# Kernel tuning notes

Hardware: AMD Instinct MI355X
Metric: run time of the kernel (lower is better)

## Reference

```python
import jax, jax.numpy as jnp
import numpy as np

N = 200_000      # n_reflns
NIMG = 500       # n_images
DMETA = 24       # metadata features
WIDTH = 32       # mlp_width
HID = 64         # hidden_units = 2*width (FeedForward default)
DEPTH = 20       # mlp_depth
NPOST = 2        # Normal posterior: (loc, scale)
EPS = 1e-12
KLW = 0.01       # scaling_kl_weight


def setup_inputs() -> dict:
    key = jax.random.key(0)
    ks = jax.random.split(key, 10)
    metadata = jax.random.normal(ks[0], (N, DMETA), jnp.float32)
    iobs = jax.random.normal(ks[1], (N, 1), jnp.float32)
    sigiobs = jax.random.uniform(ks[2], (N, 1), jnp.float32)
    image_ids = jnp.sort(jax.random.randint(ks[3], (N,), 0, NIMG)).astype(jnp.int32)
    n_reflns_per_image = jnp.bincount(image_ids, length=NIMG).astype(jnp.int32)
    d_img = DMETA + 2  # concat(metadata, iobs, sigiobs)
    w_img_in = jax.random.normal(ks[4], (d_img, WIDTH), jnp.float32) / np.float32(np.sqrt(d_img))
    b_img_in = jnp.zeros((WIDTH,), jnp.float32)
    w_scale_in = jax.random.normal(ks[5], (DMETA, WIDTH), jnp.float32) / np.float32(np.sqrt(DMETA))
    b_scale_in = jnp.zeros((WIDTH,), jnp.float32)
    # shared residual FeedForward stack (share_weights=True): x + W2 @ relu(W1 @ x)
    mlp_w1 = jax.random.normal(ks[6], (DEPTH, WIDTH, HID), jnp.float32) / np.float32(np.sqrt(WIDTH))
    mlp_b1 = jnp.zeros((DEPTH, HID), jnp.float32)
    mlp_w2 = jax.random.normal(ks[7], (DEPTH, HID, WIDTH), jnp.float32) * np.float32(0.1 / np.sqrt(HID))
    mlp_b2 = jnp.zeros((DEPTH, WIDTH), jnp.float32)
    w_out = jax.random.normal(ks[8], (WIDTH, NPOST), jnp.float32) / np.float32(np.sqrt(WIDTH))
    b_out = jnp.zeros((NPOST,), jnp.float32)
    return {
        'metadata': metadata, 'iobs': iobs, 'sigiobs': sigiobs,
        'w_img_in': w_img_in, 'b_img_in': b_img_in,
        'w_scale_in': w_scale_in, 'b_scale_in': b_scale_in,
        'mlp_w1': mlp_w1, 'mlp_b1': mlp_b1, 'mlp_w2': mlp_w2, 'mlp_b2': mlp_b2,
        'w_out': w_out, 'b_out': b_out,
        'image_ids_in_this_batch': image_ids,
        'n_reflns_per_image': n_reflns_per_image,
        'mc_samples': 32,
    }


def _mlp(h, w1, b1, w2, b2):
    # depth residual FF blocks, weights stacked along leading DEPTH axis
    def block(h, ws):
        wa, ba, wb, bb = ws
        h = h + (jax.nn.relu(h @ wa + ba) @ wb + bb)
        return h, None
    h, _ = jax.lax.scan(block, h, (w1, b1, w2, b2))
    return h


def reference(metadata, iobs, sigiobs,
              w_img_in, b_img_in, w_scale_in, b_scale_in,
              mlp_w1, mlp_b1, mlp_w2, mlp_b2, w_out, b_out,
              image_ids_in_this_batch, n_reflns_per_image, mc_samples):
    image = jnp.concatenate([metadata, iobs, sigiobs], axis=-1)   # (N, DMETA+2)
    h = image @ w_img_in + b_img_in                               # (N, W)
    h = _mlp(h, mlp_w1, mlp_b1, mlp_w2, mlp_b2)
    nimg = n_reflns_per_image.shape[0]
    sums = jax.ops.segment_sum(h, image_ids_in_this_batch, num_segments=nimg)
    counts = jnp.maximum(n_reflns_per_image, 1).astype(h.dtype)[:, None]
    pooled = sums / counts                                        # (NIMG, W) image-average pool
    s = metadata @ w_scale_in + b_scale_in + pooled[image_ids_in_this_batch]
    s = _mlp(s, mlp_w1, mlp_b1, mlp_w2, mlp_b2)                   # shared weights
    params = s @ w_out + b_out                                    # (N, 2)
    loc = params[:, 0]
    scale = jax.nn.softplus(params[:, 1]) + EPS
    # rsample from Normal(loc, scale), mc_samples draws
    noise = jax.random.normal(jax.random.key(42), (mc_samples, loc.shape[0]), loc.dtype)
    z = loc + scale * noise                                       # (S, N)
    # MC KL estimate: mean_s[log q(z) - log p(z)], p = Laplace(0, 1)
    log_q = -0.5 * jnp.square(noise) - jnp.log(scale) - np.float32(0.5 * np.log(2.0 * np.pi))
    log_p = -jnp.abs(z) - np.float32(np.log(2.0))
    kl_div = KLW * jnp.mean(log_q - log_p, axis=0)                # (N,)
    return z.T, kl_div
```

## Files before the change

### kernel.cpp

```cpp
#include <hip/hip_runtime.h>
#include <stdint.h>

#define N_ROWS 200000
#define NIMG   500
#define DMETA  24
#define WIDTH  32
#define HID    64
#define DEPTH  20
#define MC     32

#define LSTRIDE_F 68
#define TILE_F    (16 * LSTRIDE_F)

#define WB    64000
#define LSTR  17920
#define OFF_WIH (WB + DEPTH * LSTR)
#define OFF_WIL (OFF_WIH + 2048)
#define OFF_WSH (OFF_WIH + 4096)
#define OFF_WSL (OFF_WIH + 6144)

typedef __attribute__((ext_vector_type(8))) short bf16x8;
typedef __attribute__((ext_vector_type(4))) float f32x4;

#define MFMA(a, b, acc) __builtin_amdgcn_mfma_f32_16x16x32_bf16((a), (b), (acc), 0, 0, 0)

__device__ __forceinline__ uint32_t rotl32(uint32_t x, int r) {
    return (x << r) | (x >> (32 - r));
}

__device__ __forceinline__ uint32_t tf_bits(uint32_t j) {
    const uint32_t ks1 = 42u, ks2 = 0x1BD11BDAu ^ 42u;
    uint32_t x0 = 0u, x1 = j + ks1;
#define R4(a,b,c,d) \
    x0 += x1; x1 = rotl32(x1,(a)); x1 ^= x0; \
    x0 += x1; x1 = rotl32(x1,(b)); x1 ^= x0; \
    x0 += x1; x1 = rotl32(x1,(c)); x1 ^= x0; \
    x0 += x1; x1 = rotl32(x1,(d)); x1 ^= x0;
    R4(13,15,26,6)  x0 += ks1; x1 += ks2 + 1u;
    R4(17,29,16,24) x0 += ks2; x1 += 0u + 2u;
    R4(13,15,26,6)                x1 += ks1 + 3u;
    R4(17,29,16,24) x0 += ks1; x1 += ks2 + 4u;
    R4(13,15,26,6)  x0 += ks2; x1 += 0u + 5u;
#undef R4
    return x0 ^ x1;
}

__device__ __forceinline__ float bits_to_normal(uint32_t b) {
    float f = __uint_as_float((b >> 9) | 0x3f800000u) - 1.0f;
    const float lo = -0.99999994f;
    float u = fmaxf(lo, f * 2.0f + lo);
    return 1.41421356f * erfinvf(u);
}

__device__ __forceinline__ void split1(float x, short& hi, short& lo) {
    uint32_t b = __float_as_uint(x);
    uint32_t a = b + 0x8000u;
    hi = (short)(a >> 16);
    float r = x - __uint_as_float(a & 0xFFFF0000u);
    lo = (short)(__float_as_uint(r) >> 16);
}

__device__ __forceinline__ void split8p(const float* x, bf16x8& hi, bf16x8& lo) {
    uint32_t hu[4], lu[4];
#pragma unroll
    for (int p = 0; p < 4; ++p) {
        float x0 = x[2 * p], x1 = x[2 * p + 1];
        uint32_t h;
        asm("v_cvt_pk_bf16_f32 %0, %1, %2" : "=v"(h) : "v"(x0), "v"(x1));
        float r0 = x0 - __uint_as_float(h << 16);
        float r1 = x1 - __uint_as_float(h & 0xFFFF0000u);
        uint32_t l;
        asm("v_cvt_pk_bf16_f32 %0, %1, %2" : "=v"(l) : "v"(r0), "v"(r1));
        hu[p] = h;
        lu[p] = l;
    }
    __builtin_memcpy(&hi, hu, 16);
    __builtin_memcpy(&lo, lu, 16);
}

__device__ __forceinline__ void mlp20_x2(
    float* hC0, float* hC1, float* smw, const char* __restrict__ wsb,
    int lane, int q, int c) {
    const int ldsR = c * LSTRIDE_F + q * 8;
    const int ldsW = q * 4 * LSTRIDE_F + c;
    uint32_t offA  = (uint32_t)(WB + (lane << 4));
    uint32_t offB  = offA + 4096u;
    uint32_t offC  = offA + 8192u;
    uint32_t offD  = offA + 12288u;
    uint32_t offB1 = (uint32_t)(WB + 16384 + (c << 4));
    uint32_t offB2 = (uint32_t)(WB + 17408 + (c << 4));
#pragma unroll 1
    for (int l = 0; l < DEPTH; ++l) {
#pragma unroll
        for (int t = 0; t < 2; ++t)
#pragma unroll
            for (int r = 0; r < 4; ++r) {
                smw[ldsW + r * LSTRIDE_F + t * 16] = hC0[t * 4 + r];
                smw[TILE_F + ldsW + r * LSTRIDE_F + t * 16] = hC1[t * 4 + r];
            }
        f32x4 v0 = *(const f32x4*)(smw + ldsR);
        f32x4 v1 = *(const f32x4*)(smw + ldsR + 4);
        f32x4 u0 = *(const f32x4*)(smw + TILE_F + ldsR);
        f32x4 u1 = *(const f32x4*)(smw + TILE_F + ldsR + 4);
        float a0[8], a1[8];
#pragma unroll
        for (int j = 0; j < 4; ++j) {
            a0[j] = v0[j]; a0[4 + j] = v1[j];
            a1[j] = u0[j]; a1[4 + j] = u1[j];
        }
        bf16x8 ah0, al0, ah1, al1;
        split8p(a0, ah0, al0);
        split8p(a1, ah1, al1);
        float C1v0[16], C1v1[16];
#pragma unroll
        for (int t = 0; t < 4; ++t) {
            uint32_t o = (t < 2 ? offA : offB) + (uint32_t)((t & 1) << 11);
            bf16x8 bh = *(const bf16x8*)(wsb + o);
            bf16x8 bl = *(const bf16x8*)(wsb + o + 1024);
            f32x4 b1q = *(const f32x4*)(wsb + offB1 + (uint32_t)(t << 8));
            f32x4 acc = MFMA(ah0, bh, b1q);
            acc = MFMA(ah0, bl, acc); acc = MFMA(al0, bh, acc);
            f32x4 acd = MFMA(ah1, bh, b1q);
            acd = MFMA(ah1, bl, acd); acd = MFMA(al1, bh, acd);
#pragma unroll
            for (int r = 0; r < 4; ++r) {
                C1v0[t * 4 + r] = fmaxf(acc[r], 0.0f);
                C1v1[t * 4 + r] = fmaxf(acd[r], 0.0f);
            }
        }
#pragma unroll
        for (int t = 0; t < 4; ++t)
#pragma unroll
            for (int r = 0; r < 4; ++r) {
                smw[ldsW + r * LSTRIDE_F + t * 16] = C1v0[t * 4 + r];
                smw[TILE_F + ldsW + r * LSTRIDE_F + t * 16] = C1v1[t * 4 + r];
            }
        f32x4 b2q0 = *(const f32x4*)(wsb + offB2);
        f32x4 b2q1 = *(const f32x4*)(wsb + offB2 + 256u);
        f32x4 acc0[2], acc1[2];
#pragma unroll
        for (int r = 0; r < 4; ++r) {
            acc0[0][r] = hC0[r] + b2q0[r];
            acc0[1][r] = hC0[4 + r] + b2q1[r];
            acc1[0][r] = hC1[r] + b2q0[r];
            acc1[1][r] = hC1[4 + r] + b2q1[r];
        }
#pragma unroll
        for (int kf = 0; kf < 2; ++kf) {
            f32x4 e0a = *(const f32x4*)(smw + ldsR + kf * 32);
            f32x4 e0b = *(const f32x4*)(smw + ldsR + kf * 32 + 4);
            f32x4 e1a = *(const f32x4*)(smw + TILE_F + ldsR + kf * 32);
            f32x4 e1b = *(const f32x4*)(smw + TILE_F + ldsR + kf * 32 + 4);
            float e0[8], e1[8];
#pragma unroll
            for (int j = 0; j < 4; ++j) {
                e0[j] = e0a[j]; e0[4 + j] = e0b[j];
                e1[j] = e1a[j]; e1[4 + j] = e1b[j];
            }
            bf16x8 xh0, xl0, xh1, xl1;
            split8p(e0, xh0, xl0);
            split8p(e1, xh1, xl1);
#pragma unroll
            for (int t2 = 0; t2 < 2; ++t2) {
                uint32_t o = (kf ? offD : offC) + (uint32_t)(t2 << 11);
                bf16x8 bh = *(const bf16x8*)(wsb + o);
                bf16x8 bl = *(const bf16x8*)(wsb + o + 1024);
                acc0[t2] = MFMA(xh0, bh, acc0[t2]);
                acc0[t2] = MFMA(xh0, bl, acc0[t2]);
                acc0[t2] = MFMA(xl0, bh, acc0[t2]);
                acc1[t2] = MFMA(xh1, bh, acc1[t2]);
                acc1[t2] = MFMA(xh1, bl, acc1[t2]);
                acc1[t2] = MFMA(xl1, bh, acc1[t2]);
            }
        }
#pragma unroll
        for (int t2 = 0; t2 < 2; ++t2)
#pragma unroll
            for (int r = 0; r < 4; ++r) {
                hC0[t2 * 4 + r] = acc0[t2][r];
                hC1[t2 * 4 + r] = acc1[t2][r];
            }
        offA += LSTR; offB += LSTR; offC += LSTR; offD += LSTR;
        offB1 += LSTR; offB2 += LSTR;
    }
}

__device__ __forceinline__ void input_proj(
    const bf16x8& ah, const bf16x8& al, const short* __restrict__ wfh,
    const short* __restrict__ wfl, const float* __restrict__ bias,
    float* hC, int lane, int c) {
#pragma unroll
    for (int t = 0; t < 2; ++t) {
        bf16x8 bh = *(const bf16x8*)(wfh + ((t << 9) + (lane << 3)));
        bf16x8 bl = *(const bf16x8*)(wfl + ((t << 9) + (lane << 3)));
        float bb = bias[16 * t + c];
        f32x4 acc = {bb, bb, bb, bb};
        acc = MFMA(ah, bh, acc); acc = MFMA(ah, bl, acc); acc = MFMA(al, bh, acc);
#pragma unroll
        for (int r = 0; r < 4; ++r) hC[t * 4 + r] = acc[r];
    }
}

__global__ __launch_bounds__(256) void prep_kernel(
    const float* __restrict__ w1, const float* __restrict__ w2,
    const float* __restrict__ wimg, const float* __restrict__ wsc,
    const float* __restrict__ b1, const float* __restrict__ b2,
    char* __restrict__ wsb) {
    int t = blockIdx.x * 256 + threadIdx.x;
    float* sums = (float*)wsb;
    if (t < 16000) { sums[t] = 0.0f; return; }
    t -= 16000;
    if (t < 40960) {
        int l = t >> 11, r = t & 2047, tt = r >> 9, r2 = r & 511;
        int lane = r2 >> 3, j = r2 & 7;
        int k = (lane >> 4) * 8 + j, n = 16 * tt + (lane & 15);
        short h, lo;
        split1(w1[l * 2048 + k * 64 + n], h, lo);
        char* base = wsb + WB + l * LSTR + tt * 2048 + 2 * r2;
        *(short*)(base) = h;
        *(short*)(base + 1024) = lo;
        return;
    }
    t -= 40960;
    if (t < 40960) {
        int l = t >> 11, r = t & 2047, kf = r >> 10, r2 = r & 1023;
        int t2 = r2 >> 9, r3 = r2 & 511, lane = r3 >> 3, j = r3 & 7;
        int k = kf * 32 + (lane >> 4) * 8 + j, n = 16 * t2 + (lane & 15);
        short h, lo;
        split1(w2[l * 2048 + k * 32 + n], h, lo);
        char* base = wsb + WB + l * LSTR + 8192 + (kf * 2 + t2) * 2048 + 2 * r3;
        *(short*)(base) = h;
        *(short*)(base + 1024) = lo;
        return;
    }
    t -= 40960;
    if (t < 1024) {
        int tt = t >> 9, r = t & 511, lane = r >> 3, j = r & 7;
        int k = (lane >> 4) * 8 + j, n = 16 * tt + (lane & 15);
        float v = (k < 26) ? wimg[k * 32 + n] : 0.0f;
        short h, lo;
        split1(v, h, lo);
        ((short*)(wsb + OFF_WIH))[t] = h;
        ((short*)(wsb + OFF_WIL))[t] = lo;
        return;
    }
    t -= 1024;
    if (t < 1024) {
        int tt = t >> 9, r = t & 511, lane = r >> 3, j = r & 7;
        int k = (lane >> 4) * 8 + j, n = 16 * tt + (lane & 15);
        float v = (k < 24) ? wsc[k * 32 + n] : 0.0f;
        short h, lo;
        split1(v, h, lo);
        ((short*)(wsb + OFF_WSH))[t] = h;
        ((short*)(wsb + OFF_WSL))[t] = lo;
        return;
    }
    t -= 1024;
    if (t < 5120) {
        int l = t >> 8, r = t & 255;
        int tt = r >> 6, cc = (r >> 2) & 15;
        *(float*)(wsb + WB + l * LSTR + 16384 + 4 * r) = b1[l * 64 + tt * 16 + cc];
        return;
    }
    t -= 5120;
    if (t < 2560) {
        int l = t >> 7, r = t & 127;
        int t2 = r >> 6, cc = (r >> 2) & 15;
        *(float*)(wsb + WB + l * LSTR + 17408 + 4 * r) = b2[l * 32 + t2 * 16 + cc];
        return;
    }
}

__device__ __forceinline__ void load_xfrag(
    const float* __restrict__ md, const float* __restrict__ iobs,
    const float* __restrict__ sig, int base, int q, int c,
    bf16x8& ah, bf16x8& al) {
    float xa[8];
    if (q < 3) {
        const f32x4* rp = (const f32x4*)(md + (size_t)(base + c) * DMETA + q * 8);
        f32x4 v0 = rp[0], v1 = rp[1];
#pragma unroll
        for (int j = 0; j < 4; ++j) { xa[j] = v0[j]; xa[4 + j] = v1[j]; }
    } else {
        xa[0] = iobs ? iobs[base + c] : 0.0f;
        xa[1] = sig ? sig[base + c] : 0.0f;
#pragma unroll
        for (int j = 2; j < 8; ++j) xa[j] = 0.0f;
    }
    split8p(xa, ah, al);
}

__global__ __launch_bounds__(128, 4) void pass_a(
    const float* __restrict__ md, const float* __restrict__ iobs,
    const float* __restrict__ sig, const float* __restrict__ bimg,
    const char* __restrict__ wsb, const int* __restrict__ ids,
    float* __restrict__ sums) {
    __shared__ __attribute__((aligned(16))) float smat[2][2 * TILE_F];
    int lane = threadIdx.x & 63, w = threadIdx.x >> 6;
    int q = lane >> 4, c = lane & 15;
    int i0 = (blockIdx.x * 2 + w) * 32;
    float* smw = &smat[w][0];

    bf16x8 ah0, al0, ah1, al1;
    load_xfrag(md, iobs, sig, i0, q, c, ah0, al0);
    load_xfrag(md, iobs, sig, i0 + 16, q, c, ah1, al1);

    float hC0[8], hC1[8];
    input_proj(ah0, al0, (const short*)(wsb + OFF_WIH), (const short*)(wsb + OFF_WIL),
               bimg, hC0, lane, c);
    input_proj(ah1, al1, (const short*)(wsb + OFF_WIH), (const short*)(wsb + OFF_WIL),
               bimg, hC1, lane, c);

    mlp20_x2(hC0, hC1, smw, wsb, lane, q, c);

#pragma unroll
    for (int tile = 0; tile < 2; ++tile) {
        const float* hC = tile ? hC1 : hC0;
        int tb = i0 + tile * 16;
        bool uni = (ids[tb] == ids[tb + 15]);
        if (uni) {
            int id = ids[tb];
#pragma unroll
            for (int t = 0; t < 2; ++t) {
                float s = (hC[t * 4 + 0] + hC[t * 4 + 1]) + (hC[t * 4 + 2] + hC[t * 4 + 3]);
                s += __shfl_xor(s, 16, 64);
                s += __shfl_xor(s, 32, 64);
                if (q == 0) atomicAdd(&sums[id * 32 + 16 * t + c], s);
            }
        } else {
            int idv[4];
#pragma unroll
            for (int r = 0; r < 4; ++r) idv[r] = ids[tb + q * 4 + r];
#pragma unroll
            for (int t = 0; t < 2; ++t)
#pragma unroll
                for (int r = 0; r < 4; ++r)
                    atomicAdd(&sums[idv[r] * 32 + 16 * t + c], hC[t * 4 + r]);
        }
    }
}

__global__ __launch_bounds__(256) void normalize_kernel(float* __restrict__ sums,
                                                        const int* __restrict__ cnts) {
    int t = blockIdx.x * 256 + threadIdx.x;
    if (t < NIMG * WIDTH) {
        int img = t >> 5;
        float cc = (float)max(cnts[img], 1);
        sums[t] = sums[t] / cc;
    }
}

__global__ __launch_bounds__(128, 4) void pass_b(
    const float* __restrict__ md, const float* __restrict__ bsc,
    const char* __restrict__ wsb, const float* __restrict__ wout,
    const float* __restrict__ bout, const int* __restrict__ ids,
    const float* __restrict__ pooled, float* __restrict__ out) {
    __shared__ __attribute__((aligned(16))) float smat[2][2 * TILE_F];
    __shared__ float sls[2][64];
    int lane = threadIdx.x & 63, w = threadIdx.x >> 6;
    int q = lane >> 4, c = lane & 15;
    int i0 = (blockIdx.x * 2 + w) * 32;
    float* smw = &smat[w][0];

    bf16x8 ah0, al0, ah1, al1;
    load_xfrag(md, nullptr, nullptr, i0, q, c, ah0, al0);
    load_xfrag(md, nullptr, nullptr, i0 + 16, q, c, ah1, al1);

    float hC0[8], hC1[8];
    input_proj(ah0, al0, (const short*)(wsb + OFF_WSH), (const short*)(wsb + OFF_WSL),
               bsc, hC0, lane, c);
    input_proj(ah1, al1, (const short*)(wsb + OFF_WSH), (const short*)(wsb + OFF_WSL),
               bsc, hC1, lane, c);
#pragma unroll
    for (int tile = 0; tile < 2; ++tile) {
        float* hC = tile ? hC1 : hC0;
        int tb = i0 + tile * 16;
        int idv[4];
#pragma unroll
        for (int r = 0; r < 4; ++r) idv[r] = ids[tb + q * 4 + r];
#pragma unroll
        for (int t = 0; t < 2; ++t)
#pragma unroll
            for (int r = 0; r < 4; ++r)
                hC[t * 4 + r] += pooled[idv[r] * 32 + 16 * t + c];
    }

    mlp20_x2(hC0, hC1, smw, wsb, lane, q, c);

    float wo0[2], wo1[2];
#pragma unroll
    for (int t = 0; t < 2; ++t) {
        float2 wv = ((const float2*)wout)[16 * t + c];
        wo0[t] = wv.x; wo1[t] = wv.y;
    }
#pragma unroll
    for (int tile = 0; tile < 2; ++tile) {
        const float* hC = tile ? hC1 : hC0;
        float p0r[4], p1r[4];
#pragma unroll
        for (int r = 0; r < 4; ++r) {
            p0r[r] = hC[r] * wo0[0] + hC[4 + r] * wo0[1];
            p1r[r] = hC[r] * wo1[0] + hC[4 + r] * wo1[1];
        }
#pragma unroll
        for (int m = 1; m < 16; m <<= 1) {
#pragma unroll
            for (int r = 0; r < 4; ++r) {
                p0r[r] += __shfl_xor(p0r[r], m, 64);
                p1r[r] += __shfl_xor(p1r[r], m, 64);
            }
        }
        if (c == 0) {
#pragma unroll
            for (int r = 0; r < 4; ++r) {
                float loc = p0r[r] + bout[0];
                float pb = p1r[r] + bout[1];
                float scale = fmaxf(pb, 0.0f) + log1pf(expf(-fabsf(pb))) + 1e-12f;
                sls[w][tile * 16 + q * 4 + r] = loc;
                sls[w][32 + tile * 16 + q * 4 + r] = scale;
            }
        }
    }

    int ro = lane & 31, half = lane >> 5;
    int row = i0 + ro;
    float L = sls[w][ro];
    float S = sls[w][32 + ro];
    float lsg = logf(S);
    float kp = 0.0f;
    float* zrow = out + (size_t)row * MC + half * 16;
#pragma unroll 4
    for (int s4 = 0; s4 < 4; ++s4) {
        f32x4 zv;
#pragma unroll
        for (int jj = 0; jj < 4; ++jj) {
            int t = half * 16 + s4 * 4 + jj;
            uint32_t j = (uint32_t)(t * N_ROWS) + (uint32_t)row;
            float n = bits_to_normal(tf_bits(j));
            float z = fmaf(S, n, L);
            zv[jj] = z;
            kp += fmaf(-0.5f, n * n, fabsf(z));
        }
        *(f32x4*)(zrow + s4 * 4) = zv;
    }
    kp += __shfl_xor(kp, 32, 64);
    if (half == 0) {
        out[(size_t)N_ROWS * MC + row] =
            0.01f * (kp * (1.0f / 32.0f) - lsg - 0.91893853320467274f + 0.69314718055994531f);
    }
}

extern "C" void kernel_launch(void* const* d_in, const int* in_sizes, int n_in,
                              void* d_out, int out_size, void* d_ws, size_t ws_size,
                              hipStream_t stream) {
    const float* md   = (const float*)d_in[0];
    const float* iobs = (const float*)d_in[1];
    const float* sig  = (const float*)d_in[2];
    const float* wimg = (const float*)d_in[3];
    const float* bimg = (const float*)d_in[4];
    const float* wsc  = (const float*)d_in[5];
    const float* bsc  = (const float*)d_in[6];
    const float* w1   = (const float*)d_in[7];
    const float* b1   = (const float*)d_in[8];
    const float* w2   = (const float*)d_in[9];
    const float* b2   = (const float*)d_in[10];
    const float* wout = (const float*)d_in[11];
    const float* bout = (const float*)d_in[12];
    const int* ids    = (const int*)d_in[13];
    const int* cnts   = (const int*)d_in[14];
    float* out = (float*)d_out;
    char* wsb = (char*)d_ws;
    float* sums = (float*)wsb;

    const int nblk = N_ROWS / 64;
    prep_kernel<<<421, 256, 0, stream>>>(w1, w2, wimg, wsc, b1, b2, wsb);
    pass_a<<<nblk, 128, 0, stream>>>(md, iobs, sig, bimg, wsb, ids, sums);
    normalize_kernel<<<(NIMG * WIDTH + 255) / 256, 256, 0, stream>>>(sums, cnts);
    pass_b<<<nblk, 128, 0, stream>>>(md, bsc, wsb, wout, bout, ids, sums, out);
}
```

Baseline: 368.5 us.

## Switch MLP to 32x32x16 MFMA with permlane swaps, removing LDS transposes

Rewrites the 20-layer residual MLP to use 32x32x16 bf16 MFMAs, with weights as the A operand and the activations kept in registers as the B operand. Between layers the accumulator layout is rearranged into the next layer's operand layout with v_permlane32_swap instead of round-tripping through shared memory. Biases, input projections and the output projection are repacked in the prep kernel to match the new register layout. The intent is to remove the LDS store/load traffic and barriers in each layer and to cut instruction count. The trade-off is higher register pressure from the 16-float accumulators and a more fragile layout scheme, and the hidden layer is now rounded to a single bf16 (no low part) before the second matmul, which lowers precision.

```diff
diff --git a/kernel.cpp b/kernel.cpp
--- a/kernel.cpp
+++ b/kernel.cpp
@@ -9,20 +9,22 @@
 #define DEPTH  20
 #define MC     32
 
-#define LSTRIDE_F 68
-#define TILE_F    (16 * LSTRIDE_F)
-
-#define WB    64000
-#define LSTR  17920
-#define OFF_WIH (WB + DEPTH * LSTR)
-#define OFF_WIL (OFF_WIH + 2048)
-#define OFF_WSH (OFF_WIH + 4096)
-#define OFF_WSL (OFF_WIH + 6144)
+
+#define WB      64000
+#define LSTR2   16768
+#define OFF_WI  (WB + DEPTH * LSTR2)
+#define OFF_WS  (OFF_WI + 4096)
+#define OFF_BIQ (OFF_WS + 4096)
+#define OFF_BSQ (OFF_BIQ + 128)
+#define OFF_WOQ (OFF_BSQ + 128)
 
 typedef __attribute__((ext_vector_type(8))) short bf16x8;
 typedef __attribute__((ext_vector_type(4))) float f32x4;
-
-#define MFMA(a, b, acc) __builtin_amdgcn_mfma_f32_16x16x32_bf16((a), (b), (acc), 0, 0, 0)
+typedef __attribute__((ext_vector_type(16))) float f32x16;
+
+#define MFMA32(a, b, acc) __builtin_amdgcn_mfma_f32_32x32x16_bf16((a), (b), (acc), 0, 0, 0)
+#define SWP(x, y) asm("v_permlane32_swap_b32 %0, %1" : "+v"(x), "+v"(y))
+#define WOFFi(h5, reg) ((((reg) & 3) + 8 * ((reg) >> 2)) + 4 * (h5))
 
 __device__ __forceinline__ uint32_t rotl32(uint32_t x, int r) {
     return (x << r) | (x >> (32 - r));
@@ -78,265 +80,278 @@
     __builtin_memcpy(&lo, lu, 16);
 }
 
-__device__ __forceinline__ void mlp20_x2(
-    float* hC0, float* hC1, float* smw, const char* __restrict__ wsb,
-    int lane, int q, int c) {
-    const int ldsR = c * LSTRIDE_F + q * 8;
-    const int ldsW = q * 4 * LSTRIDE_F + c;
-    uint32_t offA  = (uint32_t)(WB + (lane << 4));
-    uint32_t offB  = offA + 4096u;
-    uint32_t offC  = offA + 8192u;
-    uint32_t offD  = offA + 12288u;
-    uint32_t offB1 = (uint32_t)(WB + 16384 + (c << 4));
-    uint32_t offB2 = (uint32_t)(WB + 17408 + (c << 4));
+__device__ __forceinline__ void mlp20(float* h, const char* __restrict__ wsb,
+                                      int lane, int h5) {
+    uint32_t lb = WB;
+    const uint32_t lf = (uint32_t)(lane * 16);
 #pragma unroll 1
     for (int l = 0; l < DEPTH; ++l) {
-#pragma unroll
-        for (int t = 0; t < 2; ++t)
+        uint32_t Hh[8], Hl[8];
+#pragma unroll
+        for (int p = 0; p < 8; ++p) {
+            float x0 = h[2 * p], x1 = h[2 * p + 1];
+            uint32_t wd;
+            asm("v_cvt_pk_bf16_f32 %0, %1, %2" : "=v"(wd) : "v"(x0), "v"(x1));
+            float r0 = x0 - __uint_as_float(wd << 16);
+            float r1 = x1 - __uint_as_float(wd & 0xFFFF0000u);
+            uint32_t ld;
+            asm("v_cvt_pk_bf16_f32 %0, %1, %2" : "=v"(ld) : "v"(r0), "v"(r1));
+            Hh[p] = wd;
+            Hl[p] = ld;
+        }
+        SWP(Hh[0], Hh[2]); SWP(Hh[1], Hh[3]); SWP(Hh[4], Hh[6]); SWP(Hh[5], Hh[7]);
+        SWP(Hl[0], Hl[2]); SWP(Hl[1], Hl[3]); SWP(Hl[4], Hl[6]); SWP(Hl[5], Hl[7]);
+        bf16x8 B0h, B0l, B1h, B1l;
+        __builtin_memcpy(&B0h, &Hh[0], 16);
+        __builtin_memcpy(&B1h, &Hh[4], 16);
+        __builtin_memcpy(&B0l, &Hl[0], 16);
+        __builtin_memcpy(&B1l, &Hl[4], 16);
+        uint32_t P[16];
+#pragma unroll
+        for (int tm = 0; tm < 2; ++tm) {
+            f32x16 acc;
+            {
+                const char* bq = wsb + lb + 16384u + (uint32_t)(tm * 128 + h5 * 64);
+#pragma unroll
+                for (int r = 0; r < 4; ++r) {
+                    f32x4 q = *(const f32x4*)(bq + 16 * r);
+#pragma unroll
+                    for (int i = 0; i < 4; ++i) acc[4 * r + i] = q[i];
+                }
+            }
+            const char* fa = wsb + lb + lf + (uint32_t)(tm * 4096);
+            bf16x8 a0h = *(const bf16x8*)(fa);
+            bf16x8 a0l = *(const bf16x8*)(fa + 1024);
+            bf16x8 a1h = *(const bf16x8*)(fa + 2048);
+            bf16x8 a1l = *(const bf16x8*)(fa + 3072);
+            acc = MFMA32(a0h, B0h, acc);
+            acc = MFMA32(a0h, B0l, acc);
+            acc = MFMA32(a0l, B0h, acc);
+            acc = MFMA32(a1h, B1h, acc);
+            acc = MFMA32(a1h, B1l, acc);
+            acc = MFMA32(a1l, B1h, acc);
+#pragma unroll
+            for (int p = 0; p < 8; ++p) {
+                float f0 = fmaxf(acc[2 * p], 0.0f);
+                float f1 = fmaxf(acc[2 * p + 1], 0.0f);
+                uint32_t wd;
+                asm("v_cvt_pk_bf16_f32 %0, %1, %2" : "=v"(wd) : "v"(f0), "v"(f1));
+                P[tm * 8 + p] = wd;
+            }
+        }
+        SWP(P[0], P[2]);  SWP(P[1], P[3]);  SWP(P[4], P[6]);   SWP(P[5], P[7]);
+        SWP(P[8], P[10]); SWP(P[9], P[11]); SWP(P[12], P[14]); SWP(P[13], P[15]);
+        f32x16 acc2;
+        {
+            const char* bq = wsb + lb + 16640u + (uint32_t)(h5 * 64);
 #pragma unroll
             for (int r = 0; r < 4; ++r) {
-                smw[ldsW + r * LSTRIDE_F + t * 16] = hC0[t * 4 + r];
-                smw[TILE_F + ldsW + r * LSTRIDE_F + t * 16] = hC1[t * 4 + r];
+                f32x4 q = *(const f32x4*)(bq + 16 * r);
+#pragma unroll
+                for (int i = 0; i < 4; ++i) acc2[4 * r + i] = h[4 * r + i] + q[i];
             }
-        f32x4 v0 = *(const f32x4*)(smw + ldsR);
-        f32x4 v1 = *(const f32x4*)(smw + ldsR + 4);
-        f32x4 u0 = *(const f32x4*)(smw + TILE_F + ldsR);
-        f32x4 u1 = *(const f32x4*)(smw + TILE_F + ldsR + 4);
-        float a0[8], a1[8];
-#pragma unroll
-        for (int j = 0; j < 4; ++j) {
-            a0[j] = v0[j]; a0[4 + j] = v1[j];
-            a1[j] = u0[j]; a1[4 + j] = u1[j];
-        }
-        bf16x8 ah0, al0, ah1, al1;
-        split8p(a0, ah0, al0);
-        split8p(a1, ah1, al1);
-        float C1v0[16], C1v1[16];
-#pragma unroll
-        for (int t = 0; t < 4; ++t) {
-            uint32_t o = (t < 2 ? offA : offB) + (uint32_t)((t & 1) << 11);
-            bf16x8 bh = *(const bf16x8*)(wsb + o);
-            bf16x8 bl = *(const bf16x8*)(wsb + o + 1024);
-            f32x4 b1q = *(const f32x4*)(wsb + offB1 + (uint32_t)(t << 8));
-            f32x4 acc = MFMA(ah0, bh, b1q);
-            acc = MFMA(ah0, bl, acc); acc = MFMA(al0, bh, acc);
-            f32x4 acd = MFMA(ah1, bh, b1q);
-            acd = MFMA(ah1, bl, acd); acd = MFMA(al1, bh, acd);
-#pragma unroll
-            for (int r = 0; r < 4; ++r) {
-                C1v0[t * 4 + r] = fmaxf(acc[r], 0.0f);
-                C1v1[t * 4 + r] = fmaxf(acd[r], 0.0f);
-            }
-        }
-#pragma unroll
-        for (int t = 0; t < 4; ++t)
-#pragma unroll
-            for (int r = 0; r < 4; ++r) {
-                smw[ldsW + r * LSTRIDE_F + t * 16] = C1v0[t * 4 + r];
-                smw[TILE_F + ldsW + r * LSTRIDE_F + t * 16] = C1v1[t * 4 + r];
-            }
-        f32x4 b2q0 = *(const f32x4*)(wsb + offB2);
-        f32x4 b2q1 = *(const f32x4*)(wsb + offB2 + 256u);
-        f32x4 acc0[2], acc1[2];
+        }
+#pragma unroll
+        for (int ks = 0; ks < 4; ++ks) {
+            bf16x8 Bk;
+            __builtin_memcpy(&Bk, &P[ks * 4], 16);
+            const char* fa = wsb + lb + lf + 8192u + (uint32_t)(ks * 2048);
+            bf16x8 ah = *(const bf16x8*)(fa);
+            bf16x8 al = *(const bf16x8*)(fa + 1024);
+            acc2 = MFMA32(ah, Bk, acc2);
+            acc2 = MFMA32(al, Bk, acc2);
+        }
+#pragma unroll
+        for (int i = 0; i < 16; ++i) h[i] = acc2[i];
+        lb += LSTR2;
+    }
+}
+
+__device__ __forceinline__ void input_proj32(
+    const bf16x8& x0h, const bf16x8& x0l, const bf16x8& x1h, const bf16x8& x1l,
+    const char* __restrict__ wsb, uint32_t wfoff, uint32_t bqoff,
+    float* h, int lane, int h5) {
+    f32x16 acc;
+    {
+        const char* bq = wsb + bqoff + (uint32_t)(h5 * 64);
 #pragma unroll
         for (int r = 0; r < 4; ++r) {
-            acc0[0][r] = hC0[r] + b2q0[r];
-            acc0[1][r] = hC0[4 + r] + b2q1[r];
-            acc1[0][r] = hC1[r] + b2q0[r];
-            acc1[1][r] = hC1[4 + r] + b2q1[r];
-        }
-#pragma unroll
-        for (int kf = 0; kf < 2; ++kf) {
-            f32x4 e0a = *(const f32x4*)(smw + ldsR + kf * 32);
-            f32x4 e0b = *(const f32x4*)(smw + ldsR + kf * 32 + 4);
-            f32x4 e1a = *(const f32x4*)(smw + TILE_F + ldsR + kf * 32);
-            f32x4 e1b = *(const f32x4*)(smw + TILE_F + ldsR + kf * 32 + 4);
-            float e0[8], e1[8];
-#pragma unroll
-            for (int j = 0; j < 4; ++j) {
-                e0[j] = e0a[j]; e0[4 + j] = e0b[j];
-                e1[j] = e1a[j]; e1[4 + j] = e1b[j];
-            }
-            bf16x8 xh0, xl0, xh1, xl1;
-            split8p(e0, xh0, xl0);
-            split8p(e1, xh1, xl1);
-#pragma unroll
-            for (int t2 = 0; t2 < 2; ++t2) {
-                uint32_t o = (kf ? offD : offC) + (uint32_t)(t2 << 11);
-                bf16x8 bh = *(const bf16x8*)(wsb + o);
-                bf16x8 bl = *(const bf16x8*)(wsb + o + 1024);
-                acc0[t2] = MFMA(xh0, bh, acc0[t2]);
-                acc0[t2] = MFMA(xh0, bl, acc0[t2]);
-                acc0[t2] = MFMA(xl0, bh, acc0[t2]);
-                acc1[t2] = MFMA(xh1, bh, acc1[t2]);
-                acc1[t2] = MFMA(xh1, bl, acc1[t2]);
-                acc1[t2] = MFMA(xl1, bh, acc1[t2]);
-            }
-        }
-#pragma unroll
-        for (int t2 = 0; t2 < 2; ++t2)
-#pragma unroll
-            for (int r = 0; r < 4; ++r) {
-                hC0[t2 * 4 + r] = acc0[t2][r];
-                hC1[t2 * 4 + r] = acc1[t2][r];
-            }
-        offA += LSTR; offB += LSTR; offC += LSTR; offD += LSTR;
-        offB1 += LSTR; offB2 += LSTR;
-    }
-}
-
-__device__ __forceinline__ void input_proj(
-    const bf16x8& ah, const bf16x8& al, const short* __restrict__ wfh,
-    const short* __restrict__ wfl, const float* __restrict__ bias,
-    float* hC, int lane, int c) {
-#pragma unroll
-    for (int t = 0; t < 2; ++t) {
-        bf16x8 bh = *(const bf16x8*)(wfh + ((t << 9) + (lane << 3)));
-        bf16x8 bl = *(const bf16x8*)(wfl + ((t << 9) + (lane << 3)));
-        float bb = bias[16 * t + c];
-        f32x4 acc = {bb, bb, bb, bb};
-        acc = MFMA(ah, bh, acc); acc = MFMA(ah, bl, acc); acc = MFMA(al, bh, acc);
-#pragma unroll
-        for (int r = 0; r < 4; ++r) hC[t * 4 + r] = acc[r];
-    }
+            f32x4 q = *(const f32x4*)(bq + 16 * r);
+#pragma unroll
+            for (int i = 0; i < 4; ++i) acc[4 * r + i] = q[i];
+        }
+    }
+    const char* fa = wsb + wfoff + (uint32_t)(lane * 16);
+    bf16x8 a0h = *(const bf16x8*)(fa);
+    bf16x8 a0l = *(const bf16x8*)(fa + 1024);
+    bf16x8 a1h = *(const bf16x8*)(fa + 2048);
+    bf16x8 a1l = *(const bf16x8*)(fa + 3072);
+    acc = MFMA32(a0h, x0h, acc);
+    acc = MFMA32(a0h, x0l, acc);
+    acc = MFMA32(a0l, x0h, acc);
+    acc = MFMA32(a1h, x1h, acc);
+    acc = MFMA32(a1h, x1l, acc);
+    acc = MFMA32(a1l, x1h, acc);
+#pragma unroll
+    for (int i = 0; i < 16; ++i) h[i] = acc[i];
+}
+
+__device__ __forceinline__ void load_xfrags(
+    const float* __restrict__ md, const float* __restrict__ iobs,
+    const float* __restrict__ sig, int row, int h5,
+    bf16x8& x0h, bf16x8& x0l, bf16x8& x1h, bf16x8& x1l) {
+    float xa0[8], xa1[8];
+    {
+        const f32x4* rp = (const f32x4*)(md + (size_t)row * DMETA + 8 * h5);
+        f32x4 a = rp[0], b = rp[1];
+#pragma unroll
+        for (int j = 0; j < 4; ++j) { xa0[j] = a[j]; xa0[4 + j] = b[j]; }
+    }
+    if (h5 == 0) {
+        const f32x4* rp = (const f32x4*)(md + (size_t)row * DMETA + 16);
+        f32x4 a = rp[0], b = rp[1];
+#pragma unroll
+        for (int j = 0; j < 4; ++j) { xa1[j] = a[j]; xa1[4 + j] = b[j]; }
+    } else {
+        xa1[0] = iobs ? iobs[row] : 0.0f;
+        xa1[1] = sig ? sig[row] : 0.0f;
+#pragma unroll
+        for (int j = 2; j < 8; ++j) xa1[j] = 0.0f;
+    }
+    split8p(xa0, x0h, x0l);
+    split8p(xa1, x1h, x1l);
 }
 
 __global__ __launch_bounds__(256) void prep_kernel(
     const float* __restrict__ w1, const float* __restrict__ w2,
     const float* __restrict__ wimg, const float* __restrict__ wsc,
     const float* __restrict__ b1, const float* __restrict__ b2,
-    char* __restrict__ wsb) {
+    const float* __restrict__ bimg, const float* __restrict__ bsc,
+    const float* __restrict__ wout, char* __restrict__ wsb) {
     int t = blockIdx.x * 256 + threadIdx.x;
     float* sums = (float*)wsb;
     if (t < 16000) { sums[t] = 0.0f; return; }
     t -= 16000;
     if (t < 40960) {
-        int l = t >> 11, r = t & 2047, tt = r >> 9, r2 = r & 511;
-        int lane = r2 >> 3, j = r2 & 7;
-        int k = (lane >> 4) * 8 + j, n = 16 * tt + (lane & 15);
-        short h, lo;
-        split1(w1[l * 2048 + k * 64 + n], h, lo);
-        char* base = wsb + WB + l * LSTR + tt * 2048 + 2 * r2;
-        *(short*)(base) = h;
-        *(short*)(base + 1024) = lo;
+        int l = t >> 11, r = t & 2047;
+        int tm = r >> 10, ks = (r >> 9) & 1, lane = (r >> 3) & 63, j = r & 7;
+        int k = 16 * ks + 8 * (lane >> 5) + j;
+        int u = 32 * tm + (lane & 31);
+        short hh, ll;
+        split1(w1[l * 2048 + k * 64 + u], hh, ll);
+        char* base = wsb + WB + l * LSTR2 + (tm * 2 + ks) * 2048 + 2 * (lane * 8 + j);
+        *(short*)base = hh;
+        *(short*)(base + 1024) = ll;
         return;
     }
     t -= 40960;
     if (t < 40960) {
-        int l = t >> 11, r = t & 2047, kf = r >> 10, r2 = r & 1023;
-        int t2 = r2 >> 9, r3 = r2 & 511, lane = r3 >> 3, j = r3 & 7;
-        int k = kf * 32 + (lane >> 4) * 8 + j, n = 16 * t2 + (lane & 15);
-        short h, lo;
-        split1(w2[l * 2048 + k * 32 + n], h, lo);
-        char* base = wsb + WB + l * LSTR + 8192 + (kf * 2 + t2) * 2048 + 2 * r3;
-        *(short*)(base) = h;
-        *(short*)(base + 1024) = lo;
+        int l = t >> 11, r = t & 2047;
+        int ks = r >> 9, lane = (r >> 3) & 63, j = r & 7;
+        int u = 16 * ks + 8 * (lane >> 5) + j;
+        int w = lane & 31;
+        short hh, ll;
+        split1(w2[l * 2048 + u * 32 + w], hh, ll);
+        char* base = wsb + WB + l * LSTR2 + 8192 + ks * 2048 + 2 * (lane * 8 + j);
+        *(short*)base = hh;
+        *(short*)(base + 1024) = ll;
         return;
     }
     t -= 40960;
+    if (t < 1280) {
+        int l = t >> 6, r = t & 63;
+        int tm = r >> 5, h5 = (r >> 4) & 1, reg = r & 15;
+        *(float*)(wsb + WB + l * LSTR2 + 16384 + tm * 128 + h5 * 64 + reg * 4) =
+            b1[l * 64 + 32 * tm + WOFFi(h5, reg)];
+        return;
+    }
+    t -= 1280;
+    if (t < 640) {
+        int l = t >> 5, r = t & 31;
+        int h5 = r >> 4, reg = r & 15;
+        *(float*)(wsb + WB + l * LSTR2 + 16640 + h5 * 64 + reg * 4) =
+            b2[l * 32 + WOFFi(h5, reg)];
+        return;
+    }
+    t -= 640;
     if (t < 1024) {
-        int tt = t >> 9, r = t & 511, lane = r >> 3, j = r & 7;
-        int k = (lane >> 4) * 8 + j, n = 16 * tt + (lane & 15);
-        float v = (k < 26) ? wimg[k * 32 + n] : 0.0f;
-        short h, lo;
-        split1(v, h, lo);
-        ((short*)(wsb + OFF_WIH))[t] = h;
-        ((short*)(wsb + OFF_WIL))[t] = lo;
+        int ks = t >> 9, lane = (t >> 3) & 63, j = t & 7;
+        int d = 16 * ks + 8 * (lane >> 5) + j, w = lane & 31;
+        float v = (d < 26) ? wimg[d * 32 + w] : 0.0f;
+        short hh, ll;
+        split1(v, hh, ll);
+        char* base = wsb + OFF_WI + ks * 2048 + 2 * (lane * 8 + j);
+        *(short*)base = hh;
+        *(short*)(base + 1024) = ll;
         return;
     }
     t -= 1024;
     if (t < 1024) {
-        int tt = t >> 9, r = t & 511, lane = r >> 3, j = r & 7;
-        int k = (lane >> 4) * 8 + j, n = 16 * tt + (lane & 15);
-        float v = (k < 24) ? wsc[k * 32 + n] : 0.0f;
-        short h, lo;
-        split1(v, h, lo);
-        ((short*)(wsb + OFF_WSH))[t] = h;
-        ((short*)(wsb + OFF_WSL))[t] = lo;
+        int ks = t >> 9, lane = (t >> 3) & 63, j = t & 7;
+        int d = 16 * ks + 8 * (lane >> 5) + j, w = lane & 31;
+        float v = (d < 24) ? wsc[d * 32 + w] : 0.0f;
+        short hh, ll;
+        split1(v, hh, ll);
+        char* base = wsb + OFF_WS + ks * 2048 + 2 * (lane * 8 + j);
+        *(short*)base = hh;
+        *(short*)(base + 1024) = ll;
         return;
     }
     t -= 1024;
-    if (t < 5120) {
-        int l = t >> 8, r = t & 255;
-        int tt = r >> 6, cc = (r >> 2) & 15;
-        *(float*)(wsb + WB + l * LSTR + 16384 + 4 * r) = b1[l * 64 + tt * 16 + cc];
-        return;
-    }
-    t -= 5120;
-    if (t < 2560) {
-        int l = t >> 7, r = t & 127;
-        int t2 = r >> 6, cc = (r >> 2) & 15;
-        *(float*)(wsb + WB + l * LSTR + 17408 + 4 * r) = b2[l * 32 + t2 * 16 + cc];
-        return;
-    }
-}
-
-__device__ __forceinline__ void load_xfrag(
-    const float* __restrict__ md, const float* __restrict__ iobs,
-    const float* __restrict__ sig, int base, int q, int c,
-    bf16x8& ah, bf16x8& al) {
-    float xa[8];
-    if (q < 3) {
-        const f32x4* rp = (const f32x4*)(md + (size_t)(base + c) * DMETA + q * 8);
-        f32x4 v0 = rp[0], v1 = rp[1];
-#pragma unroll
-        for (int j = 0; j < 4; ++j) { xa[j] = v0[j]; xa[4 + j] = v1[j]; }
-    } else {
-        xa[0] = iobs ? iobs[base + c] : 0.0f;
-        xa[1] = sig ? sig[base + c] : 0.0f;
-#pragma unroll
-        for (int j = 2; j < 8; ++j) xa[j] = 0.0f;
-    }
-    split8p(xa, ah, al);
+    if (t < 32) {
+        int h5 = t >> 4, reg = t & 15;
+        *(float*)(wsb + OFF_BIQ + h5 * 64 + reg * 4) = bimg[WOFFi(h5, reg)];
+        return;
+    }
+    t -= 32;
+    if (t < 32) {
+        int h5 = t >> 4, reg = t & 15;
+        *(float*)(wsb + OFF_BSQ + h5 * 64 + reg * 4) = bsc[WOFFi(h5, reg)];
+        return;
+    }
+    t -= 32;
+    if (t < 64) {
+        int h5 = t >> 5, r = t & 31, reg = r >> 1, comp = r & 1;
+        *(float*)(wsb + OFF_WOQ + h5 * 128 + reg * 8 + comp * 4) =
+            wout[WOFFi(h5, reg) * 2 + comp];
+        return;
+    }
 }
 
 __global__ __launch_bounds__(128, 4) void pass_a(
     const float* __restrict__ md, const float* __restrict__ iobs,
-    const float* __restrict__ sig, const float* __restrict__ bimg,
-    const char* __restrict__ wsb, const int* __restrict__ ids,
-    float* __restrict__ sums) {
-    __shared__ __attribute__((aligned(16))) float smat[2][2 * TILE_F];
-    int lane = threadIdx.x & 63, w = threadIdx.x >> 6;
-    int q = lane >> 4, c = lane & 15;
-    int i0 = (blockIdx.x * 2 + w) * 32;
-    float* smw = &smat[w][0];
-
-    bf16x8 ah0, al0, ah1, al1;
-    load_xfrag(md, iobs, sig, i0, q, c, ah0, al0);
-    load_xfrag(md, iobs, sig, i0 + 16, q, c, ah1, al1);
-
-    float hC0[8], hC1[8];
-    input_proj(ah0, al0, (const short*)(wsb + OFF_WIH), (const short*)(wsb + OFF_WIL),
-               bimg, hC0, lane, c);
-    input_proj(ah1, al1, (const short*)(wsb + OFF_WIH), (const short*)(wsb + OFF_WIL),
-               bimg, hC1, lane, c);
-
-    mlp20_x2(hC0, hC1, smw, wsb, lane, q, c);
-
-#pragma unroll
-    for (int tile = 0; tile < 2; ++tile) {
-        const float* hC = tile ? hC1 : hC0;
-        int tb = i0 + tile * 16;
-        bool uni = (ids[tb] == ids[tb + 15]);
-        if (uni) {
-            int id = ids[tb];
-#pragma unroll
-            for (int t = 0; t < 2; ++t) {
-                float s = (hC[t * 4 + 0] + hC[t * 4 + 1]) + (hC[t * 4 + 2] + hC[t * 4 + 3]);
-                s += __shfl_xor(s, 16, 64);
-                s += __shfl_xor(s, 32, 64);
-                if (q == 0) atomicAdd(&sums[id * 32 + 16 * t + c], s);
-            }
-        } else {
-            int idv[4];
-#pragma unroll
-            for (int r = 0; r < 4; ++r) idv[r] = ids[tb + q * 4 + r];
-#pragma unroll
-            for (int t = 0; t < 2; ++t)
-#pragma unroll
-                for (int r = 0; r < 4; ++r)
-                    atomicAdd(&sums[idv[r] * 32 + 16 * t + c], hC[t * 4 + r]);
-        }
+    const float* __restrict__ sig, const char* __restrict__ wsb,
+    const int* __restrict__ ids, float* __restrict__ sums) {
+    int lane = threadIdx.x & 63, wv = threadIdx.x >> 6;
+    int h5 = lane >> 5;
+    int R = (blockIdx.x * 2 + wv) * 32;
+    int row = R + (lane & 31);
+
+    bf16x8 x0h, x0l, x1h, x1l;
+    load_xfrags(md, iobs, sig, row, h5, x0h, x0l, x1h, x1l);
+
+    float h[16];
+    input_proj32(x0h, x0l, x1h, x1l, wsb, OFF_WI, OFF_BIQ, h, lane, h5);
+    mlp20(h, wsb, lane, h5);
+
+    int id0 = ids[R];
+    bool uni = (id0 == ids[R + 31]);
+    if (uni) {
+#pragma unroll
+        for (int m = 1; m < 32; m <<= 1) {
+#pragma unroll
+            for (int i = 0; i < 16; ++i) h[i] += __shfl_xor(h[i], m, 64);
+        }
+        if ((lane & 31) == 0) {
+#pragma unroll
+            for (int i = 0; i < 16; ++i)
+                atomicAdd(&sums[id0 * 32 + WOFFi(h5, i)], h[i]);
+        }
+    } else {
+        int id = ids[row];
+#pragma unroll
+        for (int i = 0; i < 16; ++i)
+            atomicAdd(&sums[id * 32 + WOFFi(h5, i)], h[i]);
     }
 }
 
@@ -351,100 +366,69 @@
 }
 
 __global__ __launch_bounds__(128, 4) void pass_b(
-    const float* __restrict__ md, const float* __restrict__ bsc,
-    const char* __restrict__ wsb, const float* __restrict__ wout,
+    const float* __restrict__ md, const char* __restrict__ wsb,
     const float* __restrict__ bout, const int* __restrict__ ids,
     const float* __restrict__ pooled, float* __restrict__ out) {
-    __shared__ __attribute__((aligned(16))) float smat[2][2 * TILE_F];
-    __shared__ float sls[2][64];
-    int lane = threadIdx.x & 63, w = threadIdx.x >> 6;
-    int q = lane >> 4, c = lane & 15;
-    int i0 = (blockIdx.x * 2 + w) * 32;
-    float* smw = &smat[w][0];
-
-    bf16x8 ah0, al0, ah1, al1;
-    load_xfrag(md, nullptr, nullptr, i0, q, c, ah0, al0);
-    load_xfrag(md, nullptr, nullptr, i0 + 16, q, c, ah1, al1);
-
-    float hC0[8], hC1[8];
-    input_proj(ah0, al0, (const short*)(wsb + OFF_WSH), (const short*)(wsb + OFF_WSL),
-               bsc, hC0, lane, c);
-    input_proj(ah1, al1, (const short*)(wsb + OFF_WSH), (const short*)(wsb + OFF_WSL),
-               bsc, hC1, lane, c);
-#pragma unroll
-    for (int tile = 0; tile < 2; ++tile) {
-        float* hC = tile ? hC1 : hC0;
-        int tb = i0 + tile * 16;
-        int idv[4];
-#pragma unroll
-        for (int r = 0; r < 4; ++r) idv[r] = ids[tb + q * 4 + r];
-#pragma unroll
-        for (int t = 0; t < 2; ++t)
-#pragma unroll
-            for (int r = 0; r < 4; ++r)
-                hC[t * 4 + r] += pooled[idv[r] * 32 + 16 * t + c];
-    }
-
-    mlp20_x2(hC0, hC1, smw, wsb, lane, q, c);
-
-    float wo0[2], wo1[2];
-#pragma unroll
-    for (int t = 0; t < 2; ++t) {
-        float2 wv = ((const float2*)wout)[16 * t + c];
-        wo0[t] = wv.x; wo1[t] = wv.y;
-    }
-#pragma unroll
-    for (int tile = 0; tile < 2; ++tile) {
-        const float* hC = tile ? hC1 : hC0;
-        float p0r[4], p1r[4];
-#pragma unroll
-        for (int r = 0; r < 4; ++r) {
-            p0r[r] = hC[r] * wo0[0] + hC[4 + r] * wo0[1];
-            p1r[r] = hC[r] * wo1[0] + hC[4 + r] * wo1[1];
-        }
-#pragma unroll
-        for (int m = 1; m < 16; m <<= 1) {
-#pragma unroll
-            for (int r = 0; r < 4; ++r) {
-                p0r[r] += __shfl_xor(p0r[r], m, 64);
-                p1r[r] += __shfl_xor(p1r[r], m, 64);
-            }
-        }
-        if (c == 0) {
-#pragma unroll
-            for (int r = 0; r < 4; ++r) {
-                float loc = p0r[r] + bout[0];
-                float pb = p1r[r] + bout[1];
-                float scale = fmaxf(pb, 0.0f) + log1pf(expf(-fabsf(pb))) + 1e-12f;
-                sls[w][tile * 16 + q * 4 + r] = loc;
-                sls[w][32 + tile * 16 + q * 4 + r] = scale;
-            }
-        }
-    }
-
-    int ro = lane & 31, half = lane >> 5;
-    int row = i0 + ro;
-    float L = sls[w][ro];
-    float S = sls[w][32 + ro];
-    float lsg = logf(S);
+    int lane = threadIdx.x & 63, wv = threadIdx.x >> 6;
+    int h5 = lane >> 5;
+    int R = (blockIdx.x * 2 + wv) * 32;
+    int row = R + (lane & 31);
+
+    bf16x8 x0h, x0l, x1h, x1l;
+    load_xfrags(md, nullptr, nullptr, row, h5, x0h, x0l, x1h, x1l);
+
+    float h[16];
+    input_proj32(x0h, x0l, x1h, x1l, wsb, OFF_WS, OFF_BSQ, h, lane, h5);
+
+    {
+        int idp = ids[row];
+#pragma unroll
+        for (int a = 0; a < 4; ++a) {
+            f32x4 q = *(const f32x4*)(pooled + idp * 32 + 8 * a + 4 * h5);
+#pragma unroll
+            for (int i = 0; i < 4; ++i) h[4 * a + i] += q[i];
+        }
+    }
+
+    mlp20(h, wsb, lane, h5);
+
+    float p0 = 0.0f, p1 = 0.0f;
+    {
+        const char* wq = wsb + OFF_WOQ + (uint32_t)(h5 * 128);
+#pragma unroll
+        for (int r = 0; r < 8; ++r) {
+            f32x4 q = *(const f32x4*)(wq + 16 * r);
+            p0 = fmaf(h[2 * r], q[0], p0);
+            p1 = fmaf(h[2 * r], q[1], p1);
+            p0 = fmaf(h[2 * r + 1], q[2], p0);
+            p1 = fmaf(h[2 * r + 1], q[3], p1);
+        }
+    }
+    p0 += __shfl_xor(p0, 32, 64);
+    p1 += __shfl_xor(p1, 32, 64);
+    float loc = p0 + bout[0];
+    float pb = p1 + bout[1];
+    float scale = fmaxf(pb, 0.0f) + log1pf(expf(-fabsf(pb))) + 1e-12f;
+    float lsg = logf(scale);
+
     float kp = 0.0f;
-    float* zrow = out + (size_t)row * MC + half * 16;
+    float* zrow = out + (size_t)row * MC + h5 * 16;
 #pragma unroll 4
     for (int s4 = 0; s4 < 4; ++s4) {
         f32x4 zv;
 #pragma unroll
         for (int jj = 0; jj < 4; ++jj) {
-            int t = half * 16 + s4 * 4 + jj;
-            uint32_t j = (uint32_t)(t * N_ROWS) + (uint32_t)row;
+            int tt = h5 * 16 + s4 * 4 + jj;
+            uint32_t j = (uint32_t)(tt * N_ROWS) + (uint32_t)row;
             float n = bits_to_normal(tf_bits(j));
-            float z = fmaf(S, n, L);
+            float z = fmaf(scale, n, loc);
             zv[jj] = z;
             kp += fmaf(-0.5f, n * n, fabsf(z));
         }
         *(f32x4*)(zrow + s4 * 4) = zv;
     }
     kp += __shfl_xor(kp, 32, 64);
-    if (half == 0) {
+    if (h5 == 0) {
         out[(size_t)N_ROWS * MC + row] =
             0.01f * (kp * (1.0f / 32.0f) - lsg - 0.91893853320467274f + 0.69314718055994531f);
     }
@@ -473,8 +457,8 @@
     float* sums = (float*)wsb;
 
     const int nblk = N_ROWS / 64;
-    prep_kernel<<<421, 256, 0, stream>>>(w1, w2, wimg, wsc, b1, b2, wsb);
-    pass_a<<<nblk, 128, 0, stream>>>(md, iobs, sig, bimg, wsb, ids, sums);
+    prep_kernel<<<399, 256, 0, stream>>>(w1, w2, wimg, wsc, b1, b2, bimg, bsc, wout, wsb);
+    pass_a<<<nblk, 128, 0, stream>>>(md, iobs, sig, wsb, ids, sums);
     normalize_kernel<<<(NIMG * WIDTH + 255) / 256, 256, 0, stream>>>(sums, cnts);
-    pass_b<<<nblk, 128, 0, stream>>>(md, bsc, wsb, wout, bout, ids, sums, out);
-}
+    pass_b<<<nblk, 128, 0, stream>>>(md, wsb, bout, ids, sums, out);
+}
```

Result: slower. 401.0 us (+8.8%).
